# Performance work log

Hardware: AMD Instinct MI355X
Metric: run time of the kernel (lower is better)

The kernel has to match this reference:

```python
import jax, jax.numpy as jnp
import numpy as np
import math

N = 100000      # nodes
DEG = 16        # fixed avg degree
E = N * DEG     # edges (nnz)
DIN = 128
DOUT = 32


def setup_inputs() -> dict:
    key = jax.random.key(0)
    k1, k2, k3, k4 = jax.random.split(key, 4)
    H = jax.random.normal(k1, (N, DIN), dtype=jnp.float32)
    stdv = 1.0 / math.sqrt(DOUT)
    weight = jax.random.uniform(k2, (DIN, DOUT), dtype=jnp.float32, minval=-stdv, maxval=stdv)
    # CSR adjacency: fixed degree per row -> rowPtr is an arithmetic sequence
    rowPtr = (jnp.arange(N + 1, dtype=jnp.int32) * DEG)
    colIdx = jax.random.randint(k3, (E,), 0, N, dtype=jnp.int32)
    val = jax.random.uniform(k4, (E,), dtype=jnp.float32)  # normalized edge weights
    return {"H": H, "weight": weight, "rowPtr": rowPtr, "colIdx": colIdx, "val": val}


def reference(H, weight, rowPtr, colIdx, val):
    # GCN layer: H' = A @ (H @ W), A sparse in CSR.
    HW = H @ weight                                   # [N, DOUT] dense GEMM
    n_rows = rowPtr.shape[0] - 1
    deg = jnp.diff(rowPtr)
    # expand CSR rowPtr to per-edge row ids (static total length -> jit-safe)
    rows = jnp.repeat(jnp.arange(n_rows, dtype=jnp.int32), deg,
                      total_repeat_length=colIdx.shape[0])
    msgs = HW[colIdx] * val[:, None]                  # [E, DOUT] gather + scale
    return jax.ops.segment_sum(msgs, rows, num_segments=n_rows)  # SpMM scatter-add
```

## Files before the change

### kernel.cpp

```cpp
#include <hip/hip_runtime.h>

#define DIN  128
#define DOUT 32

typedef __attribute__((ext_vector_type(8))) short bf16x8;
typedef __attribute__((ext_vector_type(4))) float f32x4;

__device__ __forceinline__ unsigned int f2b(float f) {
    unsigned int u = __float_as_uint(f);
    return (u + 0x7fffu + ((u >> 16) & 1u)) >> 16;
}
__device__ __forceinline__ unsigned int cvtpk(float lo, float hi) {
    unsigned int r;
    asm("v_cvt_pk_bf16_f32 %0, %1, %2" : "=v"(r) : "v"(lo), "v"(hi));
    return r;
}

union FragU { bf16x8 v; unsigned int u[4]; };

__device__ __forceinline__ void build_bfrag(const float* __restrict__ W,
                                            int lane, bf16x8 bfrag[2][4])
{
    const int lr = lane & 15, kh = lane >> 4;
    #pragma unroll
    for (int ct = 0; ct < 2; ++ct) {
        #pragma unroll
        for (int ks = 0; ks < 4; ++ks) {
            const int col = ct * 16 + lr;
            const int k0  = ks * 32 + kh * 8;
            float f[8];
            #pragma unroll
            for (int j = 0; j < 8; ++j) f[j] = W[(k0 + j) * DOUT + col];
            FragU fu;
            fu.u[0] = cvtpk(f[0], f[1]); fu.u[1] = cvtpk(f[2], f[3]);
            fu.u[2] = cvtpk(f[4], f[5]); fu.u[3] = cvtpk(f[6], f[7]);
            bfrag[ct][ks] = fu.v;
        }
    }
}

__device__ __forceinline__ void gemm_tile(const float* __restrict__ H,
                                          unsigned short* __restrict__ HWb,
                                          int rb, int lane,
                                          const bf16x8 bfrag[2][4])
{
    const int lr = lane & 15, kh = lane >> 4;
    const float* __restrict__ hp = H + (size_t)(rb + lr) * DIN;

    float4 raw[8];
    #pragma unroll
    for (int ks = 0; ks < 4; ++ks) {
        raw[2*ks]   = *reinterpret_cast<const float4*>(hp + ks * 32 + kh * 8);
        raw[2*ks+1] = *reinterpret_cast<const float4*>(hp + ks * 32 + kh * 8 + 4);
    }
    bf16x8 afrag[4];
    #pragma unroll
    for (int ks = 0; ks < 4; ++ks) {
        FragU fu;
        fu.u[0] = cvtpk(raw[2*ks].x,   raw[2*ks].y);
        fu.u[1] = cvtpk(raw[2*ks].z,   raw[2*ks].w);
        fu.u[2] = cvtpk(raw[2*ks+1].x, raw[2*ks+1].y);
        fu.u[3] = cvtpk(raw[2*ks+1].z, raw[2*ks+1].w);
        afrag[ks] = fu.v;
    }

    f32x4 acc[2] = {(f32x4){0.f,0.f,0.f,0.f}, (f32x4){0.f,0.f,0.f,0.f}};
    #pragma unroll
    for (int ct = 0; ct < 2; ++ct)
        #pragma unroll
        for (int ks = 0; ks < 4; ++ks)
            acc[ct] = __builtin_amdgcn_mfma_f32_16x16x32_bf16(
                afrag[ks], bfrag[ct][ks], acc[ct], 0, 0, 0);

    #pragma unroll
    for (int ct = 0; ct < 2; ++ct)
        #pragma unroll
        for (int r = 0; r < 4; ++r)
            HWb[(size_t)(rb + kh * 4 + r) * DOUT + ct * 16 + lr] =
                (unsigned short)f2b(acc[ct][r]);
}

__device__ __forceinline__ void spmm_row(const unsigned short* __restrict__ HWb,
                                         const int* __restrict__ rowPtr,
                                         const int* __restrict__ colIdx,
                                         const float* __restrict__ val,
                                         float* __restrict__ out,
                                         int n, int row, int cg)
{
    if (row >= n) return;
    const uint2* __restrict__ tbl = reinterpret_cast<const uint2*>(HWb);
    const int start = rowPtr[row];
    const int end   = rowPtr[row + 1];
    float a0 = 0.f, a1 = 0.f, a2 = 0.f, a3 = 0.f;

    #define ACC(G, V)                                                        \
        a0 = fmaf(V, __uint_as_float((G).x << 16), a0);                      \
        a1 = fmaf(V, __uint_as_float((G).x & 0xffff0000u), a1);              \
        a2 = fmaf(V, __uint_as_float((G).y << 16), a2);                      \
        a3 = fmaf(V, __uint_as_float((G).y & 0xffff0000u), a3);

    if (end - start == 16 && (start & 3) == 0) {
        const int4*   ci = reinterpret_cast<const int4*>(colIdx + start);
        const float4* vv = reinterpret_cast<const float4*>(val + start);
        const int4   c0 = ci[0], c1 = ci[1], c2 = ci[2], c3 = ci[3];
        const float4 v0 = vv[0], v1 = vv[1], v2 = vv[2], v3 = vv[3];
        const uint2 g0  = tbl[c0.x * 8 + cg], g1  = tbl[c0.y * 8 + cg];
        const uint2 g2  = tbl[c0.z * 8 + cg], g3  = tbl[c0.w * 8 + cg];
        const uint2 g4  = tbl[c1.x * 8 + cg], g5  = tbl[c1.y * 8 + cg];
        const uint2 g6  = tbl[c1.z * 8 + cg], g7  = tbl[c1.w * 8 + cg];
        const uint2 g8  = tbl[c2.x * 8 + cg], g9  = tbl[c2.y * 8 + cg];
        const uint2 g10 = tbl[c2.z * 8 + cg], g11 = tbl[c2.w * 8 + cg];
        const uint2 g12 = tbl[c3.x * 8 + cg], g13 = tbl[c3.y * 8 + cg];
        const uint2 g14 = tbl[c3.z * 8 + cg], g15 = tbl[c3.w * 8 + cg];
        ACC(g0,  v0.x) ACC(g1,  v0.y) ACC(g2,  v0.z) ACC(g3,  v0.w)
        ACC(g4,  v1.x) ACC(g5,  v1.y) ACC(g6,  v1.z) ACC(g7,  v1.w)
        ACC(g8,  v2.x) ACC(g9,  v2.y) ACC(g10, v2.z) ACC(g11, v2.w)
        ACC(g12, v3.x) ACC(g13, v3.y) ACC(g14, v3.z) ACC(g15, v3.w)
    } else {
        for (int e = start; e < end; ++e) {
            const int   c = colIdx[e];
            const float v = val[e];
            const uint2 g = tbl[c * 8 + cg];
            ACC(g, v)
        }
    }
    #undef ACC

    reinterpret_cast<float4*>(out)[(size_t)row * 8 + cg] =
        make_float4(a0, a1, a2, a3);
}

__global__ __launch_bounds__(256) void gemm_mfma_kernel(
    const float* __restrict__ H, const float* __restrict__ W,
    unsigned short* __restrict__ HWb, int n)
{
    const int lane = threadIdx.x & 63;
    const int w    = threadIdx.x >> 6;
    bf16x8 bfrag[2][4];
    build_bfrag(W, lane, bfrag);
    int rb = blockIdx.x * 64 + w * 16;
    if (rb + 16 > n) rb = n - 16;
    gemm_tile(H, HWb, rb, lane, bfrag);
}

__global__ __launch_bounds__(256) void spmm_kernel(
    const unsigned short* __restrict__ HWb, const int* __restrict__ rowPtr,
    const int* __restrict__ colIdx, const float* __restrict__ val,
    float* __restrict__ out, int n)
{
    const int gid = blockIdx.x * 256 + threadIdx.x;
    spmm_row(HWb, rowPtr, colIdx, val, out, n, gid >> 3, gid & 7);
}

__global__ __launch_bounds__(256) void fused_kernel(
    const float* __restrict__ H, const float* __restrict__ W,
    const int* __restrict__ rowPtr, const int* __restrict__ colIdx,
    const float* __restrict__ val, float* __restrict__ out, int n)
{
    __shared__ float Wlds[DIN * DOUT];
    for (int i = threadIdx.x; i < DIN * DOUT; i += 256) Wlds[i] = W[i];
    __syncthreads();

    const int gid = blockIdx.x * 256 + threadIdx.x;
    const int row = gid >> 5;
    if (row >= n) return;
    const int c = gid & 31;

    const int start = rowPtr[row];
    const int end   = rowPtr[row + 1];
    float acc = 0.f;
    for (int e = start; e < end; ++e) {
        const int   cidx = colIdx[e];
        const float v    = val[e];
        const float* h = H + (size_t)cidx * DIN;
        float dot = 0.f;
        #pragma unroll 8
        for (int k = 0; k < DIN; ++k)
            dot = fmaf(h[k], Wlds[k * DOUT + c], dot);
        acc = fmaf(v, dot, acc);
    }
    out[(size_t)row * DOUT + c] = acc;
}

extern "C" void kernel_launch(void* const* d_in, const int* in_sizes, int n_in,
                              void* d_out, int out_size, void* d_ws, size_t ws_size,
                              hipStream_t stream)
{
    const float* H      = (const float*)d_in[0];
    const float* W      = (const float*)d_in[1];
    const int*   rowPtr = (const int*)d_in[2];
    const int*   colIdx = (const int*)d_in[3];
    const float* val    = (const float*)d_in[4];
    float*       out    = (float*)d_out;

    const int n = in_sizes[2] - 1;
    const size_t hw_bytes = (size_t)n * DOUT * sizeof(unsigned short);

    if (ws_size >= hw_bytes && n >= 16) {
        unsigned short* HWb = (unsigned short*)d_ws;
        gemm_mfma_kernel<<<(n + 63) / 64, 256, 0, stream>>>(H, W, HWb, n);
        const int spmm_blocks = (int)(((size_t)n * 8 + 255) / 256);
        spmm_kernel<<<spmm_blocks, 256, 0, stream>>>(HWb, rowPtr, colIdx, val, out, n);
    } else {
        const int blocks = (int)(((size_t)n * DOUT + 255) / 256);
        fused_kernel<<<blocks, 256, 0, stream>>>(H, W, rowPtr, colIdx, val, out, n);
    }
}
```

Measured before the change: 38.08 us.

## Slice HW table into column slabs and gather 16-byte rows per thread

```diff
diff --git a/kernel.cpp b/kernel.cpp
--- a/kernel.cpp
+++ b/kernel.cpp
@@ -2,6 +2,7 @@
 
 #define DIN  128
 #define DOUT 32
+#define NSLICE 4
 
 typedef __attribute__((ext_vector_type(8))) short bf16x8;
 typedef __attribute__((ext_vector_type(4))) float f32x4;
@@ -39,11 +40,17 @@
     }
 }
 
-__device__ __forceinline__ void gemm_tile(const float* __restrict__ H,
-                                          unsigned short* __restrict__ HWb,
-                                          int rb, int lane,
-                                          const bf16x8 bfrag[2][4])
-{
+__global__ __launch_bounds__(256) void gemm_mfma_kernel(
+    const float* __restrict__ H, const float* __restrict__ W,
+    unsigned short* __restrict__ tbl16, int n)
+{
+    const int lane = threadIdx.x & 63;
+    const int w    = threadIdx.x >> 6;
+    bf16x8 bfrag[2][4];
+    build_bfrag(W, lane, bfrag);
+
+    int rb = blockIdx.x * 64 + w * 16;
+    if (rb + 16 > n) rb = n - 16;
     const int lr = lane & 15, kh = lane >> 4;
     const float* __restrict__ hp = H + (size_t)(rb + lr) * DIN;
 
@@ -73,45 +80,54 @@
                 afrag[ks], bfrag[ct][ks], acc[ct], 0, 0, 0);
 
     #pragma unroll
-    for (int ct = 0; ct < 2; ++ct)
+    for (int ct = 0; ct < 2; ++ct) {
+        const int col = ct * 16 + lr;
+        const int s   = col >> 3;
+        const int c8  = col & 7;
         #pragma unroll
-        for (int r = 0; r < 4; ++r)
-            HWb[(size_t)(rb + kh * 4 + r) * DOUT + ct * 16 + lr] =
-                (unsigned short)f2b(acc[ct][r]);
-}
-
-__device__ __forceinline__ void spmm_row(const unsigned short* __restrict__ HWb,
-                                         const int* __restrict__ rowPtr,
-                                         const int* __restrict__ colIdx,
-                                         const float* __restrict__ val,
-                                         float* __restrict__ out,
-                                         int n, int row, int cg)
-{
+        for (int r = 0; r < 4; ++r) {
+            const int row = rb + kh * 4 + r;
+            tbl16[((size_t)s * n + row) * 8 + c8] = (unsigned short)f2b(acc[ct][r]);
+        }
+    }
+}
+
+__global__ __launch_bounds__(256) void spmm_slice_kernel(
+    const unsigned short* __restrict__ tbl16, const int* __restrict__ rowPtr,
+    const int* __restrict__ colIdx, const float* __restrict__ val,
+    float* __restrict__ out, int n)
+{
+    const int s      = blockIdx.x & (NSLICE - 1);
+    const int rowblk = blockIdx.x >> 2;
+    const int row    = rowblk * 256 + threadIdx.x;
     if (row >= n) return;
-    const uint2* __restrict__ tbl = reinterpret_cast<const uint2*>(HWb);
+
+    const uint4* __restrict__ t4 =
+        reinterpret_cast<const uint4*>(tbl16) + (size_t)s * n;
+
     const int start = rowPtr[row];
     const int end   = rowPtr[row + 1];
-    float a0 = 0.f, a1 = 0.f, a2 = 0.f, a3 = 0.f;
+    float a0=0,a1=0,a2=0,a3=0,a4=0,a5=0,a6=0,a7=0;
 
     #define ACC(G, V)                                                        \
         a0 = fmaf(V, __uint_as_float((G).x << 16), a0);                      \
         a1 = fmaf(V, __uint_as_float((G).x & 0xffff0000u), a1);              \
         a2 = fmaf(V, __uint_as_float((G).y << 16), a2);                      \
-        a3 = fmaf(V, __uint_as_float((G).y & 0xffff0000u), a3);
+        a3 = fmaf(V, __uint_as_float((G).y & 0xffff0000u), a3);              \
+        a4 = fmaf(V, __uint_as_float((G).z << 16), a4);                      \
+        a5 = fmaf(V, __uint_as_float((G).z & 0xffff0000u), a5);              \
+        a6 = fmaf(V, __uint_as_float((G).w << 16), a6);                      \
+        a7 = fmaf(V, __uint_as_float((G).w & 0xffff0000u), a7);
 
     if (end - start == 16 && (start & 3) == 0) {
         const int4*   ci = reinterpret_cast<const int4*>(colIdx + start);
         const float4* vv = reinterpret_cast<const float4*>(val + start);
         const int4   c0 = ci[0], c1 = ci[1], c2 = ci[2], c3 = ci[3];
         const float4 v0 = vv[0], v1 = vv[1], v2 = vv[2], v3 = vv[3];
-        const uint2 g0  = tbl[c0.x * 8 + cg], g1  = tbl[c0.y * 8 + cg];
-        const uint2 g2  = tbl[c0.z * 8 + cg], g3  = tbl[c0.w * 8 + cg];
-        const uint2 g4  = tbl[c1.x * 8 + cg], g5  = tbl[c1.y * 8 + cg];
-        const uint2 g6  = tbl[c1.z * 8 + cg], g7  = tbl[c1.w * 8 + cg];
-        const uint2 g8  = tbl[c2.x * 8 + cg], g9  = tbl[c2.y * 8 + cg];
-        const uint2 g10 = tbl[c2.z * 8 + cg], g11 = tbl[c2.w * 8 + cg];
-        const uint2 g12 = tbl[c3.x * 8 + cg], g13 = tbl[c3.y * 8 + cg];
-        const uint2 g14 = tbl[c3.z * 8 + cg], g15 = tbl[c3.w * 8 + cg];
+        const uint4 g0  = t4[c0.x], g1  = t4[c0.y], g2  = t4[c0.z], g3  = t4[c0.w];
+        const uint4 g4  = t4[c1.x], g5  = t4[c1.y], g6  = t4[c1.z], g7  = t4[c1.w];
+        const uint4 g8  = t4[c2.x], g9  = t4[c2.y], g10 = t4[c2.z], g11 = t4[c2.w];
+        const uint4 g12 = t4[c3.x], g13 = t4[c3.y], g14 = t4[c3.z], g15 = t4[c3.w];
         ACC(g0,  v0.x) ACC(g1,  v0.y) ACC(g2,  v0.z) ACC(g3,  v0.w)
         ACC(g4,  v1.x) ACC(g5,  v1.y) ACC(g6,  v1.z) ACC(g7,  v1.w)
         ACC(g8,  v2.x) ACC(g9,  v2.y) ACC(g10, v2.z) ACC(g11, v2.w)
@@ -120,36 +136,16 @@
         for (int e = start; e < end; ++e) {
             const int   c = colIdx[e];
             const float v = val[e];
-            const uint2 g = tbl[c * 8 + cg];
+            const uint4 g = t4[c];
             ACC(g, v)
         }
     }
     #undef ACC
 
-    reinterpret_cast<float4*>(out)[(size_t)row * 8 + cg] =
-        make_float4(a0, a1, a2, a3);
-}
-
-__global__ __launch_bounds__(256) void gemm_mfma_kernel(
-    const float* __restrict__ H, const float* __restrict__ W,
-    unsigned short* __restrict__ HWb, int n)
-{
-    const int lane = threadIdx.x & 63;
-    const int w    = threadIdx.x >> 6;
-    bf16x8 bfrag[2][4];
-    build_bfrag(W, lane, bfrag);
-    int rb = blockIdx.x * 64 + w * 16;
-    if (rb + 16 > n) rb = n - 16;
-    gemm_tile(H, HWb, rb, lane, bfrag);
-}
-
-__global__ __launch_bounds__(256) void spmm_kernel(
-    const unsigned short* __restrict__ HWb, const int* __restrict__ rowPtr,
-    const int* __restrict__ colIdx, const float* __restrict__ val,
-    float* __restrict__ out, int n)
-{
-    const int gid = blockIdx.x * 256 + threadIdx.x;
-    spmm_row(HWb, rowPtr, colIdx, val, out, n, gid >> 3, gid & 7);
+    float4* __restrict__ op =
+        reinterpret_cast<float4*>(out) + (size_t)row * 8 + s * 2;
+    op[0] = make_float4(a0, a1, a2, a3);
+    op[1] = make_float4(a4, a5, a6, a7);
 }
 
 __global__ __launch_bounds__(256) void fused_kernel(
@@ -197,10 +193,11 @@
     const size_t hw_bytes = (size_t)n * DOUT * sizeof(unsigned short);
 
     if (ws_size >= hw_bytes && n >= 16) {
-        unsigned short* HWb = (unsigned short*)d_ws;
-        gemm_mfma_kernel<<<(n + 63) / 64, 256, 0, stream>>>(H, W, HWb, n);
-        const int spmm_blocks = (int)(((size_t)n * 8 + 255) / 256);
-        spmm_kernel<<<spmm_blocks, 256, 0, stream>>>(HWb, rowPtr, colIdx, val, out, n);
+        unsigned short* tbl16 = (unsigned short*)d_ws;
+        gemm_mfma_kernel<<<(n + 63) / 64, 256, 0, stream>>>(H, W, tbl16, n);
+        const int nrowblk = (n + 255) / 256;
+        spmm_slice_kernel<<<nrowblk * NSLICE, 256, 0, stream>>>(
+            tbl16, rowPtr, colIdx, val, out, n);
     } else {
         const int blocks = (int)(((size_t)n * DOUT + 255) / 256);
         fused_kernel<<<blocks, 256, 0, stream>>>(H, W, rowPtr, colIdx, val, out, n);
```

Result: slower. 55.62 us (+46.1%).
